# Performance work log

Hardware: AMD Instinct MI355X
Metric: run time of the kernel (lower is better)

## Reference

```python
import jax, jax.numpy as jnp
import numpy as np

V_MIN = -10.0
V_MAX = 10.0
N_ATOMS = 101
LN_EPS = 1e-5

B = 131072
N_OBS = 60
N_ACT = 20
H = 256


def _layer_norm(x, g, b):
    mu = jnp.mean(x, axis=-1, keepdims=True)
    var = jnp.mean(jnp.square(x - mu), axis=-1, keepdims=True)
    return (x - mu) * jax.lax.rsqrt(var + LN_EPS) * g + b


def _mlp(x, W1, b1, g1, be1, W2, b2, g2, be2, W3, b3, g3, be3, W4, b4):
    h = jax.nn.silu(_layer_norm(x @ W1 + b1, g1, be1))
    h = jax.nn.silu(_layer_norm(h @ W2 + b2, g2, be2))
    h = jax.nn.silu(_layer_norm(h @ W3 + b3, g3, be3))
    return h @ W4 + b4  # [B, N_ATOMS] logits


def setup_inputs() -> dict:
    key = jax.random.key(0)
    ks = jax.random.split(key, 10)
    s = 0.05
    return {
        'obs': jax.random.normal(ks[0], (B, N_OBS), jnp.float32),
        'actions': jax.random.normal(ks[1], (B, N_ACT), jnp.float32),
        'rewards': jax.random.normal(ks[2], (B,), jnp.float32),
        'bootstrap': jax.random.uniform(ks[3], (B,), jnp.float32),
        'discount': jax.random.uniform(ks[4], (B,), jnp.float32, 0.95, 0.99),
        'q_support': jnp.linspace(V_MIN, V_MAX, N_ATOMS, dtype=jnp.float32),
        'W1': jax.random.normal(ks[5], (N_OBS + N_ACT, H), jnp.float32) * s,
        'b1': jnp.zeros((H,), jnp.float32),
        'g1': jnp.ones((H,), jnp.float32),
        'be1': jnp.zeros((H,), jnp.float32),
        'W2': jax.random.normal(ks[6], (H, H // 2), jnp.float32) * s,
        'b2': jnp.zeros((H // 2,), jnp.float32),
        'g2': jnp.ones((H // 2,), jnp.float32),
        'be2': jnp.zeros((H // 2,), jnp.float32),
        'W3': jax.random.normal(ks[7], (H // 2, H // 4), jnp.float32) * s,
        'b3': jnp.zeros((H // 4,), jnp.float32),
        'g3': jnp.ones((H // 4,), jnp.float32),
        'be3': jnp.zeros((H // 4,), jnp.float32),
        'W4': jax.random.normal(ks[8], (H // 4, N_ATOMS), jnp.float32) * s,
        'b4': jnp.zeros((N_ATOMS,), jnp.float32),
    }


def reference(obs, actions, rewards, bootstrap, discount, q_support,
              W1, b1, g1, be1, W2, b2, g2, be2, W3, b3, g3, be3, W4, b4):
    batch = rewards.shape[0]
    delta_z = (V_MAX - V_MIN) / (N_ATOMS - 1)
    # Bellman target support: [B, N_ATOMS]
    target_z = rewards[:, None] + bootstrap[:, None] * discount[:, None] * q_support
    target_z = jnp.clip(target_z, V_MIN, V_MAX)
    b = (target_z - V_MIN) / delta_z
    li = jnp.floor(b).astype(jnp.int32)
    ui = jnp.ceil(b).astype(jnp.int32)
    is_int = ui == li
    lower_mask = is_int & (li > 0)
    upper_mask = is_int & (li == 0)
    li = jnp.where(lower_mask, li - 1, li)
    ui = jnp.where(upper_mask, ui + 1, ui)
    lf = li.astype(b.dtype)
    uf = ui.astype(b.dtype)

    x = jnp.concatenate([obs, actions], axis=-1)
    logits = _mlp(x, W1, b1, g1, be1, W2, b2, g2, be2, W3, b3, g3, be3, W4, b4)
    next_dist = jax.nn.softmax(logits, axis=1)

    size = batch * N_ATOMS
    offset = (jnp.arange(batch, dtype=jnp.int32) * N_ATOMS)[:, None]
    l_idx = jnp.clip((li + offset).reshape(-1), 0, size - 1)
    u_idx = jnp.clip((ui + offset).reshape(-1), 0, size - 1)
    lw = (next_dist * (uf - b)).reshape(-1)
    uw = (next_dist * (b - lf)).reshape(-1)
    proj = jnp.zeros((size,), next_dist.dtype).at[l_idx].add(lw).at[u_idx].add(uw)
    return proj.reshape(batch, N_ATOMS)
```

## Files before the change

### kernel.cpp

```cpp
#include <hip/hip_runtime.h>
#include <math.h>

typedef __bf16 bf16x8 __attribute__((ext_vector_type(8)));
typedef float f32x4 __attribute__((ext_vector_type(4)));

__global__ void conv_weights(const float* __restrict__ W1, const float* __restrict__ W2,
                             const float* __restrict__ W3, const float* __restrict__ W4,
                             __bf16* __restrict__ ws)
{
  const int f = blockIdx.x * 4 + (threadIdx.x >> 6);
  const int lane = threadIdx.x & 63;
  int f0, ntot, Ksrc, Nsrc, off;
  const float* W;
  if (f < 48)       { f0 = f;       ntot = 16; Ksrc = 80;  Nsrc = 256; W = W1; off = 0; }
  else if (f < 112) { f0 = f - 48;  ntot = 8;  Ksrc = 256; Nsrc = 128; W = W2; off = 24576; }
  else if (f < 128) { f0 = f - 112; ntot = 4;  Ksrc = 128; Nsrc = 64;  W = W3; off = 57344; }
  else              { f0 = f - 128; ntot = 8;  Ksrc = 64;  Nsrc = 101; W = W4; off = 65536; }
  const int kt = f0 / ntot, nt = f0 % ntot;
  const int q = lane >> 4, c = lane & 15;
  const int n = nt * 16 + c;
  bf16x8 v;
#pragma unroll
  for (int j = 0; j < 8; ++j) {
    const int k = kt * 32 + q * 8 + j;
    const float x = (k < Ksrc && n < Nsrc) ? W[k * Nsrc + n] : 0.f;
    v[j] = (__bf16)x;
  }
  ((bf16x8*)(ws + off))[f0 * 64 + lane] = v;
}


__global__ __launch_bounds__(256, 3)
void sacq_wave(const float* __restrict__ obs,  const float* __restrict__ act,
               const float* __restrict__ rew,  const float* __restrict__ boot,
               const float* __restrict__ disc, const float* __restrict__ qsup,
               const float* __restrict__ b1, const float* __restrict__ g1, const float* __restrict__ be1,
               const float* __restrict__ b2, const float* __restrict__ g2, const float* __restrict__ be2,
               const float* __restrict__ b3, const float* __restrict__ g3, const float* __restrict__ be3,
               const float* __restrict__ b4,
               const __bf16* __restrict__ ws,
               float* __restrict__ out)
{
  __shared__ float sm[13120];
  const int t = threadIdx.x;
  const int wv = t >> 6, lane = t & 63;
  const int q = lane >> 4, c = lane & 15;
  float* smw = sm + wv * 3280;
  __bf16* h1 = (__bf16*)smw;
  __bf16* h2 = (__bf16*)(smw + 2192);
  __bf16* h3 = (__bf16*)smw;
  float*  proj = smw + 576;
  const int row0w = blockIdx.x * 64 + wv * 16;
  const bf16x8* wsf = (const bf16x8*)ws;

  f32x4 acc1[16];
  {
    bf16x8 A1[3];
    const float4* ob4 = (const float4*)(obs + (size_t)(row0w + c) * 60);
    const float4* ac4 = (const float4*)(act + (size_t)(row0w + c) * 20);
#pragma unroll
    for (int kt = 0; kt < 3; ++kt) {
      const int k0 = kt * 32 + q * 8;
      float v[8];
      if (k0 < 56) {
        const float4 a = ob4[k0 / 4], b = ob4[k0 / 4 + 1];
        v[0]=a.x; v[1]=a.y; v[2]=a.z; v[3]=a.w; v[4]=b.x; v[5]=b.y; v[6]=b.z; v[7]=b.w;
      } else if (k0 == 56) {
        const float4 a = ob4[14], b = ac4[0];
        v[0]=a.x; v[1]=a.y; v[2]=a.z; v[3]=a.w; v[4]=b.x; v[5]=b.y; v[6]=b.z; v[7]=b.w;
      } else if (k0 < 80) {
        const float4 a = ac4[(k0 - 60) / 4], b = ac4[(k0 - 60) / 4 + 1];
        v[0]=a.x; v[1]=a.y; v[2]=a.z; v[3]=a.w; v[4]=b.x; v[5]=b.y; v[6]=b.z; v[7]=b.w;
      } else {
#pragma unroll
        for (int j = 0; j < 8; ++j) v[j] = 0.f;
      }
#pragma unroll
      for (int j = 0; j < 8; ++j) A1[kt][j] = (__bf16)v[j];
    }
#pragma unroll
    for (int nt = 0; nt < 16; ++nt) {
      const float bb = b1[nt * 16 + c];
      f32x4 vv = {bb, bb, bb, bb};
      acc1[nt] = vv;
    }
#pragma unroll
    for (int ch = 0; ch < 4; ++ch) {
      bf16x8 Bb[3][4];
#pragma unroll
      for (int kt = 0; kt < 3; ++kt)
#pragma unroll
        for (int j = 0; j < 4; ++j)
          Bb[kt][j] = wsf[(kt * 16 + ch * 4 + j) * 64 + lane];
#pragma unroll
      for (int kt = 0; kt < 3; ++kt)
#pragma unroll
        for (int j = 0; j < 4; ++j)
          acc1[ch * 4 + j] = __builtin_amdgcn_mfma_f32_16x16x32_bf16(A1[kt], Bb[kt][j], acc1[ch * 4 + j], 0, 0, 0);
    }
    float mu[4], rs[4];
#pragma unroll
    for (int r = 0; r < 4; ++r) {
      float s = 0.f, s2 = 0.f;
#pragma unroll
      for (int nt = 0; nt < 16; ++nt) { const float v = acc1[nt][r]; s += v; s2 += v * v; }
      s += __shfl_xor(s, 1); s2 += __shfl_xor(s2, 1);
      s += __shfl_xor(s, 2); s2 += __shfl_xor(s2, 2);
      s += __shfl_xor(s, 4); s2 += __shfl_xor(s2, 4);
      s += __shfl_xor(s, 8); s2 += __shfl_xor(s2, 8);
      const float m = s * (1.f / 256.f);
      mu[r] = m;
      rs[r] = rsqrtf(s2 * (1.f / 256.f) - m * m + 1e-5f);
    }
#pragma unroll
    for (int nt = 0; nt < 16; ++nt) {
      const int col = nt * 16 + c;
      const float gg = g1[col], bb = be1[col];
#pragma unroll
      for (int r = 0; r < 4; ++r) {
        float v = (acc1[nt][r] - mu[r]) * rs[r] * gg + bb;
        v = v * __builtin_amdgcn_rcpf(1.f + __expf(-v));
        h1[(4 * q + r) * 264 + col] = (__bf16)v;
      }
    }
  }

  {
    f32x4 acc2[8];
#pragma unroll
    for (int nt = 0; nt < 8; ++nt) {
      const float bb = b2[nt * 16 + c];
      f32x4 vv = {bb, bb, bb, bb};
      acc2[nt] = vv;
    }
    bf16x8 B2[3][8];
#pragma unroll
    for (int nt = 0; nt < 8; ++nt) B2[0][nt] = wsf[3072 + (0 * 8 + nt) * 64 + lane];
#pragma unroll
    for (int nt = 0; nt < 8; ++nt) B2[1][nt] = wsf[3072 + (1 * 8 + nt) * 64 + lane];
#pragma unroll
    for (int kt = 0; kt < 8; ++kt) {
      if (kt + 2 < 8) {
#pragma unroll
        for (int nt = 0; nt < 8; ++nt)
          B2[(kt + 2) % 3][nt] = wsf[3072 + ((kt + 2) * 8 + nt) * 64 + lane];
      }
      const bf16x8 A2 = *(const bf16x8*)(h1 + c * 264 + kt * 32 + q * 8);
#pragma unroll
      for (int nt = 0; nt < 8; ++nt)
        acc2[nt] = __builtin_amdgcn_mfma_f32_16x16x32_bf16(A2, B2[kt % 3][nt], acc2[nt], 0, 0, 0);
    }
    float mu[4], rs[4];
#pragma unroll
    for (int r = 0; r < 4; ++r) {
      float s = 0.f, s2 = 0.f;
#pragma unroll
      for (int nt = 0; nt < 8; ++nt) { const float v = acc2[nt][r]; s += v; s2 += v * v; }
      s += __shfl_xor(s, 1); s2 += __shfl_xor(s2, 1);
      s += __shfl_xor(s, 2); s2 += __shfl_xor(s2, 2);
      s += __shfl_xor(s, 4); s2 += __shfl_xor(s2, 4);
      s += __shfl_xor(s, 8); s2 += __shfl_xor(s2, 8);
      const float m = s * (1.f / 128.f);
      mu[r] = m;
      rs[r] = rsqrtf(s2 * (1.f / 128.f) - m * m + 1e-5f);
    }
#pragma unroll
    for (int nt = 0; nt < 8; ++nt) {
      const int col = nt * 16 + c;
      const float gg = g2[col], bb = be2[col];
#pragma unroll
      for (int r = 0; r < 4; ++r) {
        float v = (acc2[nt][r] - mu[r]) * rs[r] * gg + bb;
        v = v * __builtin_amdgcn_rcpf(1.f + __expf(-v));
        h2[(4 * q + r) * 136 + col] = (__bf16)v;
      }
    }
  }

  {
    bf16x8 B3[4][4];
#pragma unroll
    for (int kt = 0; kt < 4; ++kt)
#pragma unroll
      for (int nt = 0; nt < 4; ++nt)
        B3[kt][nt] = wsf[7168 + (kt * 4 + nt) * 64 + lane];
    f32x4 acc3[4];
#pragma unroll
    for (int nt = 0; nt < 4; ++nt) {
      const float bb = b3[nt * 16 + c];
      f32x4 vv = {bb, bb, bb, bb};
      acc3[nt] = vv;
    }
#pragma unroll
    for (int kt = 0; kt < 4; ++kt) {
      const bf16x8 A3 = *(const bf16x8*)(h2 + c * 136 + kt * 32 + q * 8);
#pragma unroll
      for (int nt = 0; nt < 4; ++nt)
        acc3[nt] = __builtin_amdgcn_mfma_f32_16x16x32_bf16(A3, B3[kt][nt], acc3[nt], 0, 0, 0);
    }
    float mu[4], rs[4];
#pragma unroll
    for (int r = 0; r < 4; ++r) {
      float s = 0.f, s2 = 0.f;
#pragma unroll
      for (int nt = 0; nt < 4; ++nt) { const float v = acc3[nt][r]; s += v; s2 += v * v; }
      s += __shfl_xor(s, 1); s2 += __shfl_xor(s2, 1);
      s += __shfl_xor(s, 2); s2 += __shfl_xor(s2, 2);
      s += __shfl_xor(s, 4); s2 += __shfl_xor(s2, 4);
      s += __shfl_xor(s, 8); s2 += __shfl_xor(s2, 8);
      const float m = s * (1.f / 64.f);
      mu[r] = m;
      rs[r] = rsqrtf(s2 * (1.f / 64.f) - m * m + 1e-5f);
    }
#pragma unroll
    for (int nt = 0; nt < 4; ++nt) {
      const int col = nt * 16 + c;
      const float gg = g3[col], bb = be3[col];
#pragma unroll
      for (int r = 0; r < 4; ++r) {
        float v = (acc3[nt][r] - mu[r]) * rs[r] * gg + bb;
        v = v * __builtin_amdgcn_rcpf(1.f + __expf(-v));
        h3[(4 * q + r) * 72 + col] = (__bf16)v;
      }
    }
  }

  {
    bf16x8 B4[2][7];
#pragma unroll
    for (int kt = 0; kt < 2; ++kt)
#pragma unroll
      for (int nt = 0; nt < 7; ++nt)
        B4[kt][nt] = wsf[8192 + (kt * 8 + nt) * 64 + lane];
    f32x4 a4[7];
#pragma unroll
    for (int nt = 0; nt < 7; ++nt) {
      const int col = nt * 16 + c;
      const float bb = (col < 101) ? b4[col] : 0.f;
      f32x4 vv = {bb, bb, bb, bb};
      a4[nt] = vv;
    }
#pragma unroll
    for (int kt = 0; kt < 2; ++kt) {
      const bf16x8 A4 = *(const bf16x8*)(h3 + c * 72 + kt * 32 + q * 8);
#pragma unroll
      for (int nt = 0; nt < 7; ++nt)
        a4[nt] = __builtin_amdgcn_mfma_f32_16x16x32_bf16(A4, B4[kt][nt], a4[nt], 0, 0, 0);
    }

    {
      f32x4 z = {0.f, 0.f, 0.f, 0.f};
      f32x4* p4 = (f32x4*)proj;
      for (int i = lane; i < 404; i += 64) p4[i] = z;
    }

    float mx4[4] = {-3.4e38f, -3.4e38f, -3.4e38f, -3.4e38f};
#pragma unroll
    for (int nt = 0; nt < 7; ++nt) {
      const bool ok = (nt < 6) | (c < 5);
#pragma unroll
      for (int r = 0; r < 4; ++r)
        if (ok) mx4[r] = fmaxf(mx4[r], a4[nt][r]);
    }
#pragma unroll
    for (int r = 0; r < 4; ++r) {
      mx4[r] = fmaxf(mx4[r], __shfl_xor(mx4[r], 1));
      mx4[r] = fmaxf(mx4[r], __shfl_xor(mx4[r], 2));
      mx4[r] = fmaxf(mx4[r], __shfl_xor(mx4[r], 4));
      mx4[r] = fmaxf(mx4[r], __shfl_xor(mx4[r], 8));
    }
    float sm4[4] = {0.f, 0.f, 0.f, 0.f};
#pragma unroll
    for (int nt = 0; nt < 7; ++nt) {
      const bool ok = (nt < 6) | (c < 5);
#pragma unroll
      for (int r = 0; r < 4; ++r) {
        const float e = ok ? __expf(a4[nt][r] - mx4[r]) : 0.f;
        a4[nt][r] = e;
        sm4[r] += e;
      }
    }
    float inv4[4];
#pragma unroll
    for (int r = 0; r < 4; ++r) {
      float s = sm4[r];
      s += __shfl_xor(s, 1);
      s += __shfl_xor(s, 2);
      s += __shfl_xor(s, 4);
      s += __shfl_xor(s, 8);
      inv4[r] = __builtin_amdgcn_rcpf(s);
    }

    float rwv[4], bdv[4];
#pragma unroll
    for (int r = 0; r < 4; ++r) {
      const int gr = row0w + 4 * q + r;
      rwv[r] = rew[gr];
      bdv[r] = boot[gr] * disc[gr];
    }

#pragma unroll
    for (int nt = 0; nt < 7; ++nt) {
      const int col = nt * 16 + c;
      if ((nt < 6) | (c < 5)) {
        const float qsv = qsup[col];
#pragma unroll
        for (int r = 0; r < 4; ++r) {
          const float p = a4[nt][r] * inv4[r];
          float tz = rwv[r] + bdv[r] * qsv;
          tz = fminf(fmaxf(tz, -10.f), 10.f);
          const float b_ = (tz + 10.f) * 5.f;
          const float fl = floorf(b_), cl = ceilf(b_);
          int li = (int)fl, ui = (int)cl;
          if (ui == li) { if (li > 0) --li; else ++ui; }
          const int rb = (4 * q + r) * 101;
          atomicAdd(&proj[rb + li], p * ((float)ui - b_));
          atomicAdd(&proj[rb + ui], p * (b_ - (float)li));
        }
      }
    }
  }

  {
    const f32x4* p4 = (const f32x4*)proj;
    f32x4* o4 = (f32x4*)(out + (size_t)row0w * 101);
    for (int i = lane; i < 404; i += 64) o4[i] = p4[i];
  }
}

extern "C" void kernel_launch(void* const* d_in, const int* in_sizes, int n_in,
                              void* d_out, int out_size, void* d_ws, size_t ws_size,
                              hipStream_t stream)
{
  const int B = in_sizes[2];
  __bf16* ws = (__bf16*)d_ws;

  conv_weights<<<dim3(36), dim3(256), 0, stream>>>(
      (const float*)d_in[6], (const float*)d_in[10], (const float*)d_in[14],
      (const float*)d_in[18], ws);

  sacq_wave<<<dim3(B / 64), dim3(256), 0, stream>>>(
      (const float*)d_in[0],  (const float*)d_in[1],  (const float*)d_in[2],
      (const float*)d_in[3],  (const float*)d_in[4],  (const float*)d_in[5],
      (const float*)d_in[7],  (const float*)d_in[8],  (const float*)d_in[9],
      (const float*)d_in[11], (const float*)d_in[12], (const float*)d_in[13],
      (const float*)d_in[15], (const float*)d_in[16], (const float*)d_in[17],
      (const float*)d_in[19], ws, (float*)d_out);
}
```

Before: 329.5 us.

## Switch to persistent kernel with layer weights staged in LDS

Replaces the one-block-per-64-rows launch with a persistent grid of 256 blocks that each loop over 8 tile iterations. Each block copies the packed bf16 weights W1-W3 into about 120 KB of LDS once and then reads MFMA B-fragments from LDS. Bias, gamma, beta and support vectors are hoisted into registers, and the weight packing is compacted (W1's K tail trimmed to 16, W4 to 7 column tiles). The aim is to stop re-fetching weights from global/L2 for every row tile, but the large LDS allows only one block of 4 waves per CU, which cuts occupancy and latency hiding. The batch size is now hardcoded in the launch.

```diff
diff --git a/kernel.cpp b/kernel.cpp
--- a/kernel.cpp
+++ b/kernel.cpp
@@ -10,185 +10,230 @@
 {
   const int f = blockIdx.x * 4 + (threadIdx.x >> 6);
   const int lane = threadIdx.x & 63;
-  int f0, ntot, Ksrc, Nsrc, off;
-  const float* W;
-  if (f < 48)       { f0 = f;       ntot = 16; Ksrc = 80;  Nsrc = 256; W = W1; off = 0; }
-  else if (f < 112) { f0 = f - 48;  ntot = 8;  Ksrc = 256; Nsrc = 128; W = W2; off = 24576; }
-  else if (f < 128) { f0 = f - 112; ntot = 4;  Ksrc = 128; Nsrc = 64;  W = W3; off = 57344; }
-  else              { f0 = f - 128; ntot = 8;  Ksrc = 64;  Nsrc = 101; W = W4; off = 65536; }
-  const int kt = f0 / ntot, nt = f0 % ntot;
+  if (f >= 142) return;
   const int q = lane >> 4, c = lane & 15;
-  const int n = nt * 16 + c;
   bf16x8 v;
-#pragma unroll
-  for (int j = 0; j < 8; ++j) {
-    const int k = kt * 32 + q * 8 + j;
-    const float x = (k < Ksrc && n < Nsrc) ? W[k * Nsrc + n] : 0.f;
-    v[j] = (__bf16)x;
-  }
-  ((bf16x8*)(ws + off))[f0 * 64 + lane] = v;
+  if (f < 32) {
+    const int kt = f >> 4, nt = f & 15;
+    const int n = nt * 16 + c;
+#pragma unroll
+    for (int j = 0; j < 8; ++j) v[j] = (__bf16)W1[(kt * 32 + q * 8 + j) * 256 + n];
+    *(bf16x8*)(ws + f * 512 + lane * 8) = v;
+  } else if (f < 48) {
+    if (lane < 32) {
+      const int nt = f - 32;
+      const int n = nt * 16 + c;
+#pragma unroll
+      for (int j = 0; j < 8; ++j) v[j] = (__bf16)W1[(64 + q * 8 + j) * 256 + n];
+      *(bf16x8*)(ws + 16384 + nt * 256 + lane * 8) = v;
+    }
+  } else if (f < 112) {
+    const int f0 = f - 48;
+    const int kt = f0 >> 3, nt = f0 & 7;
+    const int n = nt * 16 + c;
+#pragma unroll
+    for (int j = 0; j < 8; ++j) v[j] = (__bf16)W2[(kt * 32 + q * 8 + j) * 128 + n];
+    *(bf16x8*)(ws + 20480 + f0 * 512 + lane * 8) = v;
+  } else if (f < 128) {
+    const int f0 = f - 112;
+    const int kt = f0 >> 2, nt = f0 & 3;
+    const int n = nt * 16 + c;
+#pragma unroll
+    for (int j = 0; j < 8; ++j) v[j] = (__bf16)W3[(kt * 32 + q * 8 + j) * 64 + n];
+    *(bf16x8*)(ws + 53248 + f0 * 512 + lane * 8) = v;
+  } else {
+    const int f0 = f - 128;
+    const int kt = f0 / 7, nt = f0 % 7;
+    const int n = nt * 16 + c;
+#pragma unroll
+    for (int j = 0; j < 8; ++j)
+      v[j] = (n < 101) ? (__bf16)W4[(kt * 32 + q * 8 + j) * 101 + n] : (__bf16)0.f;
+    *(bf16x8*)(ws + 61440 + f0 * 512 + lane * 8) = v;
+  }
 }
 
 
-__global__ __launch_bounds__(256, 3)
-void sacq_wave(const float* __restrict__ obs,  const float* __restrict__ act,
-               const float* __restrict__ rew,  const float* __restrict__ boot,
-               const float* __restrict__ disc, const float* __restrict__ qsup,
-               const float* __restrict__ b1, const float* __restrict__ g1, const float* __restrict__ be1,
-               const float* __restrict__ b2, const float* __restrict__ g2, const float* __restrict__ be2,
-               const float* __restrict__ b3, const float* __restrict__ g3, const float* __restrict__ be3,
-               const float* __restrict__ b4,
-               const __bf16* __restrict__ ws,
-               float* __restrict__ out)
+__global__ __launch_bounds__(256, 1)
+void sacq_persist(const float* __restrict__ obs,  const float* __restrict__ act,
+                  const float* __restrict__ rew,  const float* __restrict__ boot,
+                  const float* __restrict__ disc, const float* __restrict__ qsup,
+                  const float* __restrict__ b1, const float* __restrict__ g1, const float* __restrict__ be1,
+                  const float* __restrict__ b2, const float* __restrict__ g2, const float* __restrict__ be2,
+                  const float* __restrict__ b3, const float* __restrict__ g3, const float* __restrict__ be3,
+                  const float* __restrict__ b4,
+                  const __bf16* __restrict__ ws,
+                  float* __restrict__ out)
 {
-  __shared__ float sm[13120];
+  __shared__ __align__(16) char smem[157952];
+  __bf16* wl = (__bf16*)smem;
   const int t = threadIdx.x;
   const int wv = t >> 6, lane = t & 63;
   const int q = lane >> 4, c = lane & 15;
-  float* smw = sm + wv * 3280;
-  __bf16* h1 = (__bf16*)smw;
-  __bf16* h2 = (__bf16*)(smw + 2192);
-  __bf16* h3 = (__bf16*)smw;
-  float*  proj = smw + 576;
-  const int row0w = blockIdx.x * 64 + wv * 16;
-  const bf16x8* wsf = (const bf16x8*)ws;
-
-  f32x4 acc1[16];
+  char* hb = smem + 122880 + wv * 8768;
+  __bf16* h1 = (__bf16*)hb;
+  __bf16* h2 = (__bf16*)hb;
+  __bf16* h3 = (__bf16*)hb;
+  float*  proj = (float*)(hb + 2304);
+
   {
+    const uint4* src = (const uint4*)ws;
+    uint4* dst = (uint4*)smem;
+    for (int i = t; i < 7680; i += 256) dst[i] = src[i];
+  }
+
+  float b1v[16], g1v[16], be1v[16];
+#pragma unroll
+  for (int nt = 0; nt < 16; ++nt) {
+    const int col = nt * 16 + c;
+    b1v[nt] = b1[col]; g1v[nt] = g1[col]; be1v[nt] = be1[col];
+  }
+  float b2v[8], g2v[8], be2v[8];
+#pragma unroll
+  for (int nt = 0; nt < 8; ++nt) {
+    const int col = nt * 16 + c;
+    b2v[nt] = b2[col]; g2v[nt] = g2[col]; be2v[nt] = be2[col];
+  }
+  float b3v[4], g3v[4], be3v[4];
+#pragma unroll
+  for (int nt = 0; nt < 4; ++nt) {
+    const int col = nt * 16 + c;
+    b3v[nt] = b3[col]; g3v[nt] = g3[col]; be3v[nt] = be3[col];
+  }
+  float b4v[7], qsv[7];
+#pragma unroll
+  for (int nt = 0; nt < 7; ++nt) {
+    const int col = nt * 16 + c;
+    b4v[nt] = (col < 101) ? b4[col] : 0.f;
+    qsv[nt] = (col < 101) ? qsup[col] : 0.f;
+  }
+  bf16x8 B4[2][7];
+#pragma unroll
+  for (int kt = 0; kt < 2; ++kt)
+#pragma unroll
+    for (int nt = 0; nt < 7; ++nt)
+      B4[kt][nt] = *(const bf16x8*)(ws + 61440 + (kt * 7 + nt) * 512 + lane * 8);
+
+  __syncthreads();
+
+  for (int it = 0; it < 8; ++it) {
+    const int tile = it * 1024 + blockIdx.x * 4 + wv;
+    const int row0 = tile * 16;
+
     bf16x8 A1[3];
-    const float4* ob4 = (const float4*)(obs + (size_t)(row0w + c) * 60);
-    const float4* ac4 = (const float4*)(act + (size_t)(row0w + c) * 20);
-#pragma unroll
-    for (int kt = 0; kt < 3; ++kt) {
-      const int k0 = kt * 32 + q * 8;
-      float v[8];
-      if (k0 < 56) {
-        const float4 a = ob4[k0 / 4], b = ob4[k0 / 4 + 1];
-        v[0]=a.x; v[1]=a.y; v[2]=a.z; v[3]=a.w; v[4]=b.x; v[5]=b.y; v[6]=b.z; v[7]=b.w;
-      } else if (k0 == 56) {
-        const float4 a = ob4[14], b = ac4[0];
-        v[0]=a.x; v[1]=a.y; v[2]=a.z; v[3]=a.w; v[4]=b.x; v[5]=b.y; v[6]=b.z; v[7]=b.w;
-      } else if (k0 < 80) {
-        const float4 a = ac4[(k0 - 60) / 4], b = ac4[(k0 - 60) / 4 + 1];
-        v[0]=a.x; v[1]=a.y; v[2]=a.z; v[3]=a.w; v[4]=b.x; v[5]=b.y; v[6]=b.z; v[7]=b.w;
-      } else {
-#pragma unroll
-        for (int j = 0; j < 8; ++j) v[j] = 0.f;
-      }
-#pragma unroll
-      for (int j = 0; j < 8; ++j) A1[kt][j] = (__bf16)v[j];
-    }
+    {
+      const float4* ob4 = (const float4*)(obs + (size_t)(row0 + c) * 60);
+      const float4* ac4 = (const float4*)(act + (size_t)(row0 + c) * 20);
+#pragma unroll
+      for (int kt = 0; kt < 3; ++kt) {
+        const int k0 = kt * 32 + q * 8;
+        float v[8];
+        if (k0 < 56) {
+          const float4 a = ob4[k0 / 4], b = ob4[k0 / 4 + 1];
+          v[0]=a.x; v[1]=a.y; v[2]=a.z; v[3]=a.w; v[4]=b.x; v[5]=b.y; v[6]=b.z; v[7]=b.w;
+        } else if (k0 == 56) {
+          const float4 a = ob4[14], b = ac4[0];
+          v[0]=a.x; v[1]=a.y; v[2]=a.z; v[3]=a.w; v[4]=b.x; v[5]=b.y; v[6]=b.z; v[7]=b.w;
+        } else if (k0 < 80) {
+          const float4 a = ac4[(k0 - 60) / 4], b = ac4[(k0 - 60) / 4 + 1];
+          v[0]=a.x; v[1]=a.y; v[2]=a.z; v[3]=a.w; v[4]=b.x; v[5]=b.y; v[6]=b.z; v[7]=b.w;
+        } else {
+#pragma unroll
+          for (int j = 0; j < 8; ++j) v[j] = 0.f;
+        }
+#pragma unroll
+        for (int j = 0; j < 8; ++j) A1[kt][j] = (__bf16)v[j];
+      }
+    }
+
+    f32x4 acc1[16];
 #pragma unroll
     for (int nt = 0; nt < 16; ++nt) {
-      const float bb = b1[nt * 16 + c];
-      f32x4 vv = {bb, bb, bb, bb};
+      f32x4 vv = {b1v[nt], b1v[nt], b1v[nt], b1v[nt]};
       acc1[nt] = vv;
     }
 #pragma unroll
-    for (int ch = 0; ch < 4; ++ch) {
-      bf16x8 Bb[3][4];
-#pragma unroll
-      for (int kt = 0; kt < 3; ++kt)
-#pragma unroll
-        for (int j = 0; j < 4; ++j)
-          Bb[kt][j] = wsf[(kt * 16 + ch * 4 + j) * 64 + lane];
-#pragma unroll
-      for (int kt = 0; kt < 3; ++kt)
-#pragma unroll
-        for (int j = 0; j < 4; ++j)
-          acc1[ch * 4 + j] = __builtin_amdgcn_mfma_f32_16x16x32_bf16(A1[kt], Bb[kt][j], acc1[ch * 4 + j], 0, 0, 0);
-    }
-    float mu[4], rs[4];
-#pragma unroll
-    for (int r = 0; r < 4; ++r) {
-      float s = 0.f, s2 = 0.f;
-#pragma unroll
-      for (int nt = 0; nt < 16; ++nt) { const float v = acc1[nt][r]; s += v; s2 += v * v; }
-      s += __shfl_xor(s, 1); s2 += __shfl_xor(s2, 1);
-      s += __shfl_xor(s, 2); s2 += __shfl_xor(s2, 2);
-      s += __shfl_xor(s, 4); s2 += __shfl_xor(s2, 4);
-      s += __shfl_xor(s, 8); s2 += __shfl_xor(s2, 8);
-      const float m = s * (1.f / 256.f);
-      mu[r] = m;
-      rs[r] = rsqrtf(s2 * (1.f / 256.f) - m * m + 1e-5f);
-    }
-#pragma unroll
-    for (int nt = 0; nt < 16; ++nt) {
-      const int col = nt * 16 + c;
-      const float gg = g1[col], bb = be1[col];
+    for (int kt = 0; kt < 2; ++kt)
+#pragma unroll
+      for (int nt = 0; nt < 16; ++nt)
+        acc1[nt] = __builtin_amdgcn_mfma_f32_16x16x32_bf16(
+            A1[kt], *(const bf16x8*)(wl + (kt * 16 + nt) * 512 + lane * 8), acc1[nt], 0, 0, 0);
+#pragma unroll
+    for (int nt = 0; nt < 16; ++nt)
+      acc1[nt] = __builtin_amdgcn_mfma_f32_16x16x32_bf16(
+          A1[2], *(const bf16x8*)(wl + 16384 + nt * 256 + (lane & 31) * 8), acc1[nt], 0, 0, 0);
+
+    {
+      float mu[4], rs[4];
 #pragma unroll
       for (int r = 0; r < 4; ++r) {
-        float v = (acc1[nt][r] - mu[r]) * rs[r] * gg + bb;
-        v = v * __builtin_amdgcn_rcpf(1.f + __expf(-v));
-        h1[(4 * q + r) * 264 + col] = (__bf16)v;
-      }
-    }
-  }
-
-  {
+        float s = 0.f, s2 = 0.f;
+#pragma unroll
+        for (int nt = 0; nt < 16; ++nt) { const float v = acc1[nt][r]; s += v; s2 += v * v; }
+        s += __shfl_xor(s, 1); s2 += __shfl_xor(s2, 1);
+        s += __shfl_xor(s, 2); s2 += __shfl_xor(s2, 2);
+        s += __shfl_xor(s, 4); s2 += __shfl_xor(s2, 4);
+        s += __shfl_xor(s, 8); s2 += __shfl_xor(s2, 8);
+        const float m = s * (1.f / 256.f);
+        mu[r] = m;
+        rs[r] = rsqrtf(s2 * (1.f / 256.f) - m * m + 1e-5f);
+      }
+#pragma unroll
+      for (int nt = 0; nt < 16; ++nt) {
+        const int col = nt * 16 + c;
+#pragma unroll
+        for (int r = 0; r < 4; ++r) {
+          float v = (acc1[nt][r] - mu[r]) * rs[r] * g1v[nt] + be1v[nt];
+          v = v * __builtin_amdgcn_rcpf(1.f + __expf(-v));
+          h1[(4 * q + r) * 264 + col] = (__bf16)v;
+        }
+      }
+    }
+
     f32x4 acc2[8];
 #pragma unroll
     for (int nt = 0; nt < 8; ++nt) {
-      const float bb = b2[nt * 16 + c];
-      f32x4 vv = {bb, bb, bb, bb};
+      f32x4 vv = {b2v[nt], b2v[nt], b2v[nt], b2v[nt]};
       acc2[nt] = vv;
     }
-    bf16x8 B2[3][8];
-#pragma unroll
-    for (int nt = 0; nt < 8; ++nt) B2[0][nt] = wsf[3072 + (0 * 8 + nt) * 64 + lane];
-#pragma unroll
-    for (int nt = 0; nt < 8; ++nt) B2[1][nt] = wsf[3072 + (1 * 8 + nt) * 64 + lane];
 #pragma unroll
     for (int kt = 0; kt < 8; ++kt) {
-      if (kt + 2 < 8) {
-#pragma unroll
-        for (int nt = 0; nt < 8; ++nt)
-          B2[(kt + 2) % 3][nt] = wsf[3072 + ((kt + 2) * 8 + nt) * 64 + lane];
-      }
       const bf16x8 A2 = *(const bf16x8*)(h1 + c * 264 + kt * 32 + q * 8);
 #pragma unroll
       for (int nt = 0; nt < 8; ++nt)
-        acc2[nt] = __builtin_amdgcn_mfma_f32_16x16x32_bf16(A2, B2[kt % 3][nt], acc2[nt], 0, 0, 0);
-    }
-    float mu[4], rs[4];
-#pragma unroll
-    for (int r = 0; r < 4; ++r) {
-      float s = 0.f, s2 = 0.f;
-#pragma unroll
-      for (int nt = 0; nt < 8; ++nt) { const float v = acc2[nt][r]; s += v; s2 += v * v; }
-      s += __shfl_xor(s, 1); s2 += __shfl_xor(s2, 1);
-      s += __shfl_xor(s, 2); s2 += __shfl_xor(s2, 2);
-      s += __shfl_xor(s, 4); s2 += __shfl_xor(s2, 4);
-      s += __shfl_xor(s, 8); s2 += __shfl_xor(s2, 8);
-      const float m = s * (1.f / 128.f);
-      mu[r] = m;
-      rs[r] = rsqrtf(s2 * (1.f / 128.f) - m * m + 1e-5f);
-    }
-#pragma unroll
-    for (int nt = 0; nt < 8; ++nt) {
-      const int col = nt * 16 + c;
-      const float gg = g2[col], bb = be2[col];
+        acc2[nt] = __builtin_amdgcn_mfma_f32_16x16x32_bf16(
+            A2, *(const bf16x8*)(wl + 20480 + (kt * 8 + nt) * 512 + lane * 8), acc2[nt], 0, 0, 0);
+    }
+    {
+      float mu[4], rs[4];
 #pragma unroll
       for (int r = 0; r < 4; ++r) {
-        float v = (acc2[nt][r] - mu[r]) * rs[r] * gg + bb;
-        v = v * __builtin_amdgcn_rcpf(1.f + __expf(-v));
-        h2[(4 * q + r) * 136 + col] = (__bf16)v;
-      }
-    }
-  }
-
-  {
-    bf16x8 B3[4][4];
-#pragma unroll
-    for (int kt = 0; kt < 4; ++kt)
-#pragma unroll
-      for (int nt = 0; nt < 4; ++nt)
-        B3[kt][nt] = wsf[7168 + (kt * 4 + nt) * 64 + lane];
+        float s = 0.f, s2 = 0.f;
+#pragma unroll
+        for (int nt = 0; nt < 8; ++nt) { const float v = acc2[nt][r]; s += v; s2 += v * v; }
+        s += __shfl_xor(s, 1); s2 += __shfl_xor(s2, 1);
+        s += __shfl_xor(s, 2); s2 += __shfl_xor(s2, 2);
+        s += __shfl_xor(s, 4); s2 += __shfl_xor(s2, 4);
+        s += __shfl_xor(s, 8); s2 += __shfl_xor(s2, 8);
+        const float m = s * (1.f / 128.f);
+        mu[r] = m;
+        rs[r] = rsqrtf(s2 * (1.f / 128.f) - m * m + 1e-5f);
+      }
+#pragma unroll
+      for (int nt = 0; nt < 8; ++nt) {
+        const int col = nt * 16 + c;
+#pragma unroll
+        for (int r = 0; r < 4; ++r) {
+          float v = (acc2[nt][r] - mu[r]) * rs[r] * g2v[nt] + be2v[nt];
+          v = v * __builtin_amdgcn_rcpf(1.f + __expf(-v));
+          h2[(4 * q + r) * 136 + col] = (__bf16)v;
+        }
+      }
+    }
+
     f32x4 acc3[4];
 #pragma unroll
     for (int nt = 0; nt < 4; ++nt) {
-      const float bb = b3[nt * 16 + c];
-      f32x4 vv = {bb, bb, bb, bb};
+      f32x4 vv = {b3v[nt], b3v[nt], b3v[nt], b3v[nt]};
       acc3[nt] = vv;
     }
 #pragma unroll
@@ -196,48 +241,40 @@
       const bf16x8 A3 = *(const bf16x8*)(h2 + c * 136 + kt * 32 + q * 8);
 #pragma unroll
       for (int nt = 0; nt < 4; ++nt)
-        acc3[nt] = __builtin_amdgcn_mfma_f32_16x16x32_bf16(A3, B3[kt][nt], acc3[nt], 0, 0, 0);
-    }
-    float mu[4], rs[4];
-#pragma unroll
-    for (int r = 0; r < 4; ++r) {
-      float s = 0.f, s2 = 0.f;
-#pragma unroll
-      for (int nt = 0; nt < 4; ++nt) { const float v = acc3[nt][r]; s += v; s2 += v * v; }
-      s += __shfl_xor(s, 1); s2 += __shfl_xor(s2, 1);
-      s += __shfl_xor(s, 2); s2 += __shfl_xor(s2, 2);
-      s += __shfl_xor(s, 4); s2 += __shfl_xor(s2, 4);
-      s += __shfl_xor(s, 8); s2 += __shfl_xor(s2, 8);
-      const float m = s * (1.f / 64.f);
-      mu[r] = m;
-      rs[r] = rsqrtf(s2 * (1.f / 64.f) - m * m + 1e-5f);
-    }
-#pragma unroll
-    for (int nt = 0; nt < 4; ++nt) {
-      const int col = nt * 16 + c;
-      const float gg = g3[col], bb = be3[col];
+        acc3[nt] = __builtin_amdgcn_mfma_f32_16x16x32_bf16(
+            A3, *(const bf16x8*)(wl + 53248 + (kt * 4 + nt) * 512 + lane * 8), acc3[nt], 0, 0, 0);
+    }
+    {
+      float mu[4], rs[4];
 #pragma unroll
       for (int r = 0; r < 4; ++r) {
-        float v = (acc3[nt][r] - mu[r]) * rs[r] * gg + bb;
-        v = v * __builtin_amdgcn_rcpf(1.f + __expf(-v));
-        h3[(4 * q + r) * 72 + col] = (__bf16)v;
-      }
-    }
-  }
-
-  {
-    bf16x8 B4[2][7];
-#pragma unroll
-    for (int kt = 0; kt < 2; ++kt)
-#pragma unroll
-      for (int nt = 0; nt < 7; ++nt)
-        B4[kt][nt] = wsf[8192 + (kt * 8 + nt) * 64 + lane];
+        float s = 0.f, s2 = 0.f;
+#pragma unroll
+        for (int nt = 0; nt < 4; ++nt) { const float v = acc3[nt][r]; s += v; s2 += v * v; }
+        s += __shfl_xor(s, 1); s2 += __shfl_xor(s2, 1);
+        s += __shfl_xor(s, 2); s2 += __shfl_xor(s2, 2);
+        s += __shfl_xor(s, 4); s2 += __shfl_xor(s2, 4);
+        s += __shfl_xor(s, 8); s2 += __shfl_xor(s2, 8);
+        const float m = s * (1.f / 64.f);
+        mu[r] = m;
+        rs[r] = rsqrtf(s2 * (1.f / 64.f) - m * m + 1e-5f);
+      }
+#pragma unroll
+      for (int nt = 0; nt < 4; ++nt) {
+        const int col = nt * 16 + c;
+#pragma unroll
+        for (int r = 0; r < 4; ++r) {
+          float v = (acc3[nt][r] - mu[r]) * rs[r] * g3v[nt] + be3v[nt];
+          v = v * __builtin_amdgcn_rcpf(1.f + __expf(-v));
+          h3[(4 * q + r) * 72 + col] = (__bf16)v;
+        }
+      }
+    }
+
     f32x4 a4[7];
 #pragma unroll
     for (int nt = 0; nt < 7; ++nt) {
-      const int col = nt * 16 + c;
-      const float bb = (col < 101) ? b4[col] : 0.f;
-      f32x4 vv = {bb, bb, bb, bb};
+      f32x4 vv = {b4v[nt], b4v[nt], b4v[nt], b4v[nt]};
       a4[nt] = vv;
     }
 #pragma unroll
@@ -253,7 +290,6 @@
       f32x4* p4 = (f32x4*)proj;
       for (int i = lane; i < 404; i += 64) p4[i] = z;
     }
-
     float mx4[4] = {-3.4e38f, -3.4e38f, -3.4e38f, -3.4e38f};
 #pragma unroll
     for (int nt = 0; nt < 7; ++nt) {
@@ -290,24 +326,21 @@
       s += __shfl_xor(s, 8);
       inv4[r] = __builtin_amdgcn_rcpf(s);
     }
-
     float rwv[4], bdv[4];
 #pragma unroll
     for (int r = 0; r < 4; ++r) {
-      const int gr = row0w + 4 * q + r;
+      const int gr = row0 + 4 * q + r;
       rwv[r] = rew[gr];
       bdv[r] = boot[gr] * disc[gr];
     }
-
 #pragma unroll
     for (int nt = 0; nt < 7; ++nt) {
-      const int col = nt * 16 + c;
       if ((nt < 6) | (c < 5)) {
-        const float qsv = qsup[col];
+        const float qsvv = qsv[nt];
 #pragma unroll
         for (int r = 0; r < 4; ++r) {
           const float p = a4[nt][r] * inv4[r];
-          float tz = rwv[r] + bdv[r] * qsv;
+          float tz = rwv[r] + bdv[r] * qsvv;
           tz = fminf(fmaxf(tz, -10.f), 10.f);
           const float b_ = (tz + 10.f) * 5.f;
           const float fl = floorf(b_), cl = ceilf(b_);
@@ -319,12 +352,12 @@
         }
       }
     }
-  }
-
-  {
-    const f32x4* p4 = (const f32x4*)proj;
-    f32x4* o4 = (f32x4*)(out + (size_t)row0w * 101);
-    for (int i = lane; i < 404; i += 64) o4[i] = p4[i];
+
+    {
+      const f32x4* p4 = (const f32x4*)proj;
+      f32x4* o4 = (f32x4*)(out + (size_t)row0 * 101);
+      for (int i = lane; i < 404; i += 64) o4[i] = p4[i];
+    }
   }
 }
 
@@ -332,14 +365,13 @@
                               void* d_out, int out_size, void* d_ws, size_t ws_size,
                               hipStream_t stream)
 {
-  const int B = in_sizes[2];
   __bf16* ws = (__bf16*)d_ws;
 
   conv_weights<<<dim3(36), dim3(256), 0, stream>>>(
       (const float*)d_in[6], (const float*)d_in[10], (const float*)d_in[14],
       (const float*)d_in[18], ws);
 
-  sacq_wave<<<dim3(B / 64), dim3(256), 0, stream>>>(
+  sacq_persist<<<dim3(256), dim3(256), 0, stream>>>(
       (const float*)d_in[0],  (const float*)d_in[1],  (const float*)d_in[2],
       (const float*)d_in[3],  (const float*)d_in[4],  (const float*)d_in[5],
       (const float*)d_in[7],  (const float*)d_in[8],  (const float*)d_in[9],
```

Measured after the change: 365.6 us. +11.0%, slower.
